# Kernel tuning notes

Measured on AMD Instinct MI355X. Metric: run time of the kernel, lower is better.

The kernel has to match this reference:

```python
import jax, jax.numpy as jnp
import numpy as np

IOU_THR = 0.5
SIGMA = 0.2
BETA = 0.6
EPS = 1e-8
SCORE_FLOOR = 0.01
N_BOXES = 8192
IMG = 640.0


def setup_inputs() -> dict:
    key = jax.random.key(0)
    k1, k2, k3 = jax.random.split(key, 3)
    # realistic detector output: centers in [0, 640], sizes in [5, 105]
    c = jax.random.uniform(k1, (N_BOXES, 2), dtype=jnp.float32) * IMG
    wh = jax.random.uniform(k2, (N_BOXES, 2), dtype=jnp.float32) * 100.0 + 5.0
    boxes = jnp.concatenate([c - wh / 2, c + wh / 2], axis=-1)  # [N,4] x1y1x2y2
    scores = jax.random.uniform(k3, (N_BOXES,), dtype=jnp.float32)
    return {"boxes": boxes, "scores": scores}


def pairwise_iou(b):
    # b: [N,4] -> [N,N]
    x1 = jnp.maximum(b[:, None, 0], b[None, :, 0])
    y1 = jnp.maximum(b[:, None, 1], b[None, :, 1])
    x2 = jnp.minimum(b[:, None, 2], b[None, :, 2])
    y2 = jnp.minimum(b[:, None, 3], b[None, :, 3])
    inter = jnp.clip(x2 - x1, 0) * jnp.clip(y2 - y1, 0)
    area = (b[:, 2] - b[:, 0]) * (b[:, 3] - b[:, 1])
    union = area[:, None] + area[None, :] - inter
    return inter / (union + EPS)


def diou_vec(b1, B):
    # b1: [4] pseudo-box, B: [N,4] pseudo-boxes -> DIoU [N]
    # (faithful to original: calculate_diou is called on rows of the IoU matrix,
    #  which only uses the first 4 columns as if they were box coords)
    x1 = jnp.maximum(b1[0], B[:, 0]); y1 = jnp.maximum(b1[1], B[:, 1])
    x2 = jnp.minimum(b1[2], B[:, 2]); y2 = jnp.minimum(b1[3], B[:, 3])
    inter = jnp.clip(x2 - x1, 0) * jnp.clip(y2 - y1, 0)
    a1 = (b1[2] - b1[0]) * (b1[3] - b1[1])
    a2 = (B[:, 2] - B[:, 0]) * (B[:, 3] - B[:, 1])
    iou = inter / (a1 + a2 - inter + EPS)
    cx1 = (b1[0] + b1[2]) / 2; cy1 = (b1[1] + b1[3]) / 2
    cx2 = (B[:, 0] + B[:, 2]) / 2; cy2 = (B[:, 1] + B[:, 3]) / 2
    cdist = (cx1 - cx2) ** 2 + (cy1 - cy2) ** 2
    ex1 = jnp.minimum(b1[0], B[:, 0]); ey1 = jnp.minimum(b1[1], B[:, 1])
    ex2 = jnp.maximum(b1[2], B[:, 2]); ey2 = jnp.maximum(b1[3], B[:, 3])
    edist = (ex2 - ex1) ** 2 + (ey2 - ey1) ** 2
    return iou - cdist / (edist + EPS)


def reference(boxes, scores):
    n = boxes.shape[0]
    order = jnp.argsort(-scores)              # descending score order
    b = boxes[order]
    s = scores[order]
    iou = pairwise_iou(b)                     # [N,N]
    iou_triu = iou * jnp.triu(jnp.ones((n, n), iou.dtype), k=1)
    pseudo = iou[:, :4]                       # rows of IoU matrix used as "boxes" (as in original)

    def body(carry, xs):
        keep, sc = carry
        row_triu, pbox, i = xs
        row_keep = keep[i]                    # skip row if already suppressed
        suppress = (row_triu > IOU_THR) & keep
        penalty = jnp.exp(-(row_triu ** 2) / SIGMA)
        diou = diou_vec(pbox, pseudo)
        total = jnp.minimum(penalty + diou ** 2 / BETA, 1.0)
        active = row_keep & suppress
        new_sc = jnp.where(active, sc * total, sc)
        new_keep = keep & ~(active & (new_sc < SCORE_FLOOR))
        return (new_keep, new_sc), None

    init = (jnp.ones(n, dtype=bool), s)
    (keep, sc), _ = jax.lax.scan(body, init, (iou_triu, pseudo, jnp.arange(n)))

    # map back to original index order
    scores_out = jnp.zeros_like(scores).at[order].set(sc)
    keep_out = jnp.zeros(n, dtype=bool).at[order].set(keep)
    return scores_out, keep_out
```

## Files before the change

### kernel.cpp

```cpp
#include <hip/hip_runtime.h>

#define N 8192
#define IOU_THR 0.5f
#define SIGMA 0.2f
#define BETA 0.6f
#define EPSF 1e-8f
#define SCORE_FLOOR 0.01f
#define NMS_T 1024
#define MAXS 20
#define PAIR_BUF 2048

__device__ __forceinline__ float iou_f(float4 a, float4 b) {
    float x1 = fmaxf(a.x, b.x);
    float y1 = fmaxf(a.y, b.y);
    float x2 = fminf(a.z, b.z);
    float y2 = fminf(a.w, b.w);
    float inter = fmaxf(x2 - x1, 0.0f) * fmaxf(y2 - y1, 0.0f);
    float aa = (a.z - a.x) * (a.w - a.y);
    float ab = (b.z - b.x) * (b.w - b.y);
    return inter / (aa + ab - inter + EPSF);
}

__device__ __forceinline__ float diou_f(float4 a, float4 b) {
    float x1 = fmaxf(a.x, b.x);
    float y1 = fmaxf(a.y, b.y);
    float x2 = fminf(a.z, b.z);
    float y2 = fminf(a.w, b.w);
    float inter = fmaxf(x2 - x1, 0.0f) * fmaxf(y2 - y1, 0.0f);
    float a1 = (a.z - a.x) * (a.w - a.y);
    float a2 = (b.z - b.x) * (b.w - b.y);
    float iou = inter / (a1 + a2 - inter + EPSF);
    float cx1 = (a.x + a.z) * 0.5f, cy1 = (a.y + a.w) * 0.5f;
    float cx2 = (b.x + b.z) * 0.5f, cy2 = (b.y + b.w) * 0.5f;
    float dx = cx1 - cx2, dy = cy1 - cy2;
    float cdist = dx * dx + dy * dy;
    float ex1 = fminf(a.x, b.x), ey1 = fminf(a.y, b.y);
    float ex2 = fmaxf(a.z, b.z), ey2 = fmaxf(a.w, b.w);
    float ew = ex2 - ex1, eh = ey2 - ey1;
    float edist = ew * ew + eh * eh;
    return iou - cdist / (edist + EPSF);
}

__global__ __launch_bounds__(256) void k_rank(const float* __restrict__ scores,
                                              int* __restrict__ rank) {
    __shared__ unsigned long long kj[256];
    int tid = threadIdx.x;
    int gj = blockIdx.x * 256 + tid;
    unsigned sbj = __float_as_uint(scores[gj]);
    kj[tid] = ((unsigned long long)(~sbj) << 32) | (unsigned)gj;
    __syncthreads();
    int gi = blockIdx.y * 256 + tid;
    unsigned sbi = __float_as_uint(scores[gi]);
    unsigned long long ki = ((unsigned long long)(~sbi) << 32) | (unsigned)gi;
    int cnt = 0;
#pragma unroll 8
    for (int q = 0; q < 256; ++q) cnt += (kj[q] < ki) ? 1 : 0;
    if (cnt) atomicAdd(&rank[gi], cnt);
}

__global__ __launch_bounds__(256) void k_scatter(const float4* __restrict__ boxes,
                                                 const float* __restrict__ scores,
                                                 const int* __restrict__ rank,
                                                 int* __restrict__ order,
                                                 float* __restrict__ s_sorted,
                                                 float4* __restrict__ b_sorted) {
    int t = blockIdx.x * 256 + threadIdx.x;
    int r = rank[t];
    order[r] = t;
    s_sorted[r] = scores[t];
    b_sorted[r] = boxes[t];
}

__global__ __launch_bounds__(256) void k_pairs(const float4* __restrict__ b,
                                               int* __restrict__ counter,
                                               int2* __restrict__ adj, int cap) {
    int tj = blockIdx.x, ti = blockIdx.y;
    if (tj < ti) return;
    __shared__ float4 bj[256];
    __shared__ float4 pj[256];
    __shared__ int2 lbuf[PAIR_BUF];
    __shared__ int lcount;
    __shared__ int lbase;
    int tid = threadIdx.x;
    if (tid == 0) lcount = 0;
    float4 t0 = b[0], t1 = b[1], t2 = b[2], t3 = b[3];
    int jbase = tj * 256;
    float4 bjv = b[jbase + tid];
    bj[tid] = bjv;
    float4 pjv;
    pjv.x = iou_f(bjv, t0);
    pjv.y = iou_f(bjv, t1);
    pjv.z = iou_f(bjv, t2);
    pjv.w = iou_f(bjv, t3);
    pj[tid] = pjv;
    __syncthreads();
    int i = ti * 256 + tid;
    float4 bi = b[i];
    float4 pi;
    pi.x = iou_f(bi, t0);
    pi.y = iou_f(bi, t1);
    pi.z = iou_f(bi, t2);
    pi.w = iou_f(bi, t3);
    for (int jj = 0; jj < 256; ++jj) {
        int j = jbase + jj;
        if (j <= i) continue;
        float v = iou_f(bi, bj[jj]);
        if (v > IOU_THR) {
            float penalty = expf(-(v * v) / SIGMA);
            float d = diou_f(pi, pj[jj]);
            float total = fminf(penalty + (d * d) / BETA, 1.0f);
            int pos = atomicAdd(&lcount, 1);
            if (pos < PAIR_BUF) {
                int2 e;
                e.x = (i << 13) | j;
                e.y = __float_as_int(total);
                lbuf[pos] = e;
            }
        }
    }
    __syncthreads();
    if (tid == 0) {
        int c = lcount;
        if (c > PAIR_BUF) c = PAIR_BUF;
        lcount = c;
        lbase = (c > 0) ? atomicAdd(counter, c) : 0;
    }
    __syncthreads();
    int c = lcount, base = lbase;
    for (int t = tid; t < c; t += 256) {
        int slot = base + t;
        if (slot < cap) adj[slot] = lbuf[t];
    }
}

__global__ __launch_bounds__(NMS_T) void k_nms(const int2* __restrict__ adj,
                                               const int* __restrict__ counter,
                                               const float* __restrict__ s_sorted,
                                               const int* __restrict__ order,
                                               float* __restrict__ out, int cap) {
    __shared__ float sc_l[N];
    __shared__ unsigned char keep_l[N];
    __shared__ unsigned int tag[N];
    int tid = threadIdx.x;
    for (int r = tid; r < N; r += NMS_T) {
        sc_l[r] = s_sorted[r];
        keep_l[r] = 1;
        tag[r] = 0u;
    }
    int T = counter[0];
    if (T > cap) T = cap;
    unsigned int ij[MAXS];
    float tot[MAXS];
    unsigned int mask = 0u;
#pragma unroll
    for (int s = 0; s < MAXS; ++s) {
        int g = s * NMS_T + tid;
        if (g < T) {
            int2 e = adj[g];
            ij[s] = (unsigned)e.x;
            tot[s] = __int_as_float(e.y);
            mask |= 1u << s;
        } else {
            ij[s] = 0u;
            tot[s] = 0.0f;
        }
    }
    unsigned int step = 0u;
    while (__syncthreads_count((int)(mask != 0u))) {
        ++step;
        unsigned int sv = step << 13;
#pragma unroll
        for (int s = 0; s < MAXS; ++s) {
            if (mask & (1u << s)) {
                unsigned int j_ = ij[s] & 8191u;
                unsigned int i_ = ij[s] >> 13;
                atomicMax(&tag[j_], sv | (8191u - i_));
            }
        }
        __syncthreads();
#pragma unroll
        for (int s = 0; s < MAXS; ++s) {
            if (mask & (1u << s)) {
                unsigned int i_ = ij[s] >> 13;
                unsigned int j_ = ij[s] & 8191u;
                unsigned int tgi = tag[i_];
                unsigned int tgj = tag[j_];
                if (((tgi >> 13) != step) && (tgj == (sv | (8191u - i_)))) {
                    if (keep_l[i_] && keep_l[j_]) {
                        float ns = sc_l[j_] * tot[s];
                        sc_l[j_] = ns;
                        if (ns < SCORE_FLOOR) keep_l[j_] = 0;
                    }
                    mask &= ~(1u << s);
                }
            }
        }
    }
    for (int r = tid; r < N; r += NMS_T) {
        int oi = order[r];
        out[oi] = sc_l[r];
        out[N + oi] = keep_l[r] ? 1.0f : 0.0f;
    }
}

extern "C" void kernel_launch(void* const* d_in, const int* in_sizes, int n_in,
                              void* d_out, int out_size, void* d_ws, size_t ws_size,
                              hipStream_t stream) {
    const float4* boxes = (const float4*)d_in[0];
    const float* scores = (const float*)d_in[1];
    float* out = (float*)d_out;
    char* ws = (char*)d_ws;

    int* order = (int*)(ws);
    float* s_sorted = (float*)(ws + (32 << 10));
    float4* b_sorted = (float4*)(ws + (64 << 10));
    int* rank = (int*)(ws + (192 << 10));
    int* counter = (int*)(ws + (224 << 10));
    int2* adj = (int2*)(ws + (256 << 10));

    long long cap_ll = ((long long)ws_size - (256 << 10)) / 8;
    if (cap_ll < 0) cap_ll = 0;
    if (cap_ll > (long long)NMS_T * MAXS) cap_ll = (long long)NMS_T * MAXS;
    int cap = (int)cap_ll;

    hipMemsetAsync(ws + (192 << 10), 0, 64 << 10, stream);
    hipLaunchKernelGGL(k_rank, dim3(32, 32), dim3(256), 0, stream, scores, rank);
    hipLaunchKernelGGL(k_scatter, dim3(32), dim3(256), 0, stream, boxes, scores, rank,
                       order, s_sorted, b_sorted);
    hipLaunchKernelGGL(k_pairs, dim3(32, 32), dim3(256), 0, stream, b_sorted, counter, adj, cap);
    hipLaunchKernelGGL(k_nms, dim3(1), dim3(NMS_T), 0, stream, adj, counter, s_sorted, order, out, cap);
}
```

Before: 215.2 us.

## Fuse rank, scatter, pair and NMS stages into one cooperative kernel

Replaces the memset and four separate launches with a single cooperative kernel of 256 blocks of 512 threads. Stages are separated by grid-wide syncs, and the upper-triangular tile pairs are enumerated with a linear index so that no block sits idle. The NMS phase now runs in one 512-thread block with up to 40 pair slots per thread, and it re-reads pair entries from global memory each step instead of holding them in registers. This removes launch and memset overhead, at the cost of grid-sync latency, a smaller NMS block, and extra global loads inside the serial NMS loop.

```diff
diff --git a/kernel.cpp b/kernel.cpp
--- a/kernel.cpp
+++ b/kernel.cpp
@@ -1,4 +1,7 @@
 #include <hip/hip_runtime.h>
+#include <hip/hip_cooperative_groups.h>
+
+namespace cg = cooperative_groups;
 
 #define N 8192
 #define IOU_THR 0.5f
@@ -6,8 +9,10 @@
 #define BETA 0.6f
 #define EPSF 1e-8f
 #define SCORE_FLOOR 0.01f
-#define NMS_T 1024
-#define MAXS 20
+#define NBLK 256
+#define NTHR 512
+#define MAXS 40
+#define CAP (NTHR * MAXS)
 #define PAIR_BUF 2048
 
 __device__ __forceinline__ float iou_f(float4 a, float4 b) {
@@ -41,165 +46,170 @@
     return iou - cdist / (edist + EPSF);
 }
 
-__global__ __launch_bounds__(256) void k_rank(const float* __restrict__ scores,
-                                              int* __restrict__ rank) {
-    __shared__ unsigned long long kj[256];
+__global__ __launch_bounds__(NTHR) void k_fused(const float4* __restrict__ boxes,
+                                                const float* __restrict__ scores,
+                                                float* __restrict__ out,
+                                                int* __restrict__ rank,
+                                                int* __restrict__ order,
+                                                float* __restrict__ s_sorted,
+                                                float4* __restrict__ b_sorted,
+                                                int2* __restrict__ adj, int cap) {
+    cg::grid_group grid = cg::this_grid();
+    __shared__ __align__(16) char smem[73728];
+    __shared__ int lcount, lbase;
     int tid = threadIdx.x;
-    int gj = blockIdx.x * 256 + tid;
-    unsigned sbj = __float_as_uint(scores[gj]);
-    kj[tid] = ((unsigned long long)(~sbj) << 32) | (unsigned)gj;
-    __syncthreads();
-    int gi = blockIdx.y * 256 + tid;
-    unsigned sbi = __float_as_uint(scores[gi]);
-    unsigned long long ki = ((unsigned long long)(~sbi) << 32) | (unsigned)gi;
-    int cnt = 0;
+    int b = blockIdx.x;
+
+    {
+        int idx = b * NTHR + tid;
+        if (idx <= N) rank[idx] = 0;
+    }
+    grid.sync();
+
+    {
+        unsigned long long* kj = (unsigned long long*)smem;
+        int it = b >> 4, jt = b & 15;
+        int gj = jt * NTHR + tid;
+        unsigned sbj = __float_as_uint(scores[gj]);
+        kj[tid] = ((unsigned long long)(~sbj) << 32) | (unsigned)gj;
+        __syncthreads();
+        int gi = it * NTHR + tid;
+        unsigned sbi = __float_as_uint(scores[gi]);
+        unsigned long long ki = ((unsigned long long)(~sbi) << 32) | (unsigned)gi;
+        int cnt = 0;
 #pragma unroll 8
-    for (int q = 0; q < 256; ++q) cnt += (kj[q] < ki) ? 1 : 0;
-    if (cnt) atomicAdd(&rank[gi], cnt);
-}
-
-__global__ __launch_bounds__(256) void k_scatter(const float4* __restrict__ boxes,
-                                                 const float* __restrict__ scores,
-                                                 const int* __restrict__ rank,
-                                                 int* __restrict__ order,
-                                                 float* __restrict__ s_sorted,
-                                                 float4* __restrict__ b_sorted) {
-    int t = blockIdx.x * 256 + threadIdx.x;
-    int r = rank[t];
-    order[r] = t;
-    s_sorted[r] = scores[t];
-    b_sorted[r] = boxes[t];
-}
-
-__global__ __launch_bounds__(256) void k_pairs(const float4* __restrict__ b,
-                                               int* __restrict__ counter,
-                                               int2* __restrict__ adj, int cap) {
-    int tj = blockIdx.x, ti = blockIdx.y;
-    if (tj < ti) return;
-    __shared__ float4 bj[256];
-    __shared__ float4 pj[256];
-    __shared__ int2 lbuf[PAIR_BUF];
-    __shared__ int lcount;
-    __shared__ int lbase;
-    int tid = threadIdx.x;
-    if (tid == 0) lcount = 0;
-    float4 t0 = b[0], t1 = b[1], t2 = b[2], t3 = b[3];
-    int jbase = tj * 256;
-    float4 bjv = b[jbase + tid];
-    bj[tid] = bjv;
-    float4 pjv;
-    pjv.x = iou_f(bjv, t0);
-    pjv.y = iou_f(bjv, t1);
-    pjv.z = iou_f(bjv, t2);
-    pjv.w = iou_f(bjv, t3);
-    pj[tid] = pjv;
-    __syncthreads();
-    int i = ti * 256 + tid;
-    float4 bi = b[i];
-    float4 pi;
-    pi.x = iou_f(bi, t0);
-    pi.y = iou_f(bi, t1);
-    pi.z = iou_f(bi, t2);
-    pi.w = iou_f(bi, t3);
-    for (int jj = 0; jj < 256; ++jj) {
-        int j = jbase + jj;
-        if (j <= i) continue;
-        float v = iou_f(bi, bj[jj]);
-        if (v > IOU_THR) {
-            float penalty = expf(-(v * v) / SIGMA);
-            float d = diou_f(pi, pj[jj]);
-            float total = fminf(penalty + (d * d) / BETA, 1.0f);
-            int pos = atomicAdd(&lcount, 1);
-            if (pos < PAIR_BUF) {
-                int2 e;
-                e.x = (i << 13) | j;
-                e.y = __float_as_int(total);
-                lbuf[pos] = e;
-            }
-        }
-    }
-    __syncthreads();
-    if (tid == 0) {
-        int c = lcount;
-        if (c > PAIR_BUF) c = PAIR_BUF;
-        lcount = c;
-        lbase = (c > 0) ? atomicAdd(counter, c) : 0;
-    }
-    __syncthreads();
-    int c = lcount, base = lbase;
-    for (int t = tid; t < c; t += 256) {
-        int slot = base + t;
-        if (slot < cap) adj[slot] = lbuf[t];
-    }
-}
-
-__global__ __launch_bounds__(NMS_T) void k_nms(const int2* __restrict__ adj,
-                                               const int* __restrict__ counter,
-                                               const float* __restrict__ s_sorted,
-                                               const int* __restrict__ order,
-                                               float* __restrict__ out, int cap) {
-    __shared__ float sc_l[N];
-    __shared__ unsigned char keep_l[N];
-    __shared__ unsigned int tag[N];
-    int tid = threadIdx.x;
-    for (int r = tid; r < N; r += NMS_T) {
-        sc_l[r] = s_sorted[r];
-        keep_l[r] = 1;
-        tag[r] = 0u;
-    }
-    int T = counter[0];
-    if (T > cap) T = cap;
-    unsigned int ij[MAXS];
-    float tot[MAXS];
-    unsigned int mask = 0u;
+        for (int q = 0; q < NTHR; ++q) cnt += (kj[q] < ki) ? 1 : 0;
+        if (cnt) atomicAdd(&rank[gi], cnt);
+        __syncthreads();
+    }
+    grid.sync();
+
+    if (b < 16) {
+        int t = b * NTHR + tid;
+        int r = rank[t];
+        order[r] = t;
+        s_sorted[r] = scores[t];
+        b_sorted[r] = boxes[t];
+    }
+    grid.sync();
+
+    {
+        float4* bj = (float4*)smem;
+        float4* pj = (float4*)(smem + 4096);
+        int2* lbuf = (int2*)(smem + 8192);
+        float4 t0 = b_sorted[0], t1 = b_sorted[1], t2 = b_sorted[2], t3 = b_sorted[3];
+        for (int L = b; L < 528; L += NBLK) {
+            int ti = 0, off = 0;
+            while (off + (32 - ti) <= L) { off += 32 - ti; ++ti; }
+            int tj = ti + (L - off);
+            __syncthreads();
+            if (tid == 0) lcount = 0;
+            if (tid < 256) {
+                float4 bv = b_sorted[tj * 256 + tid];
+                bj[tid] = bv;
+                float4 pv;
+                pv.x = iou_f(bv, t0); pv.y = iou_f(bv, t1);
+                pv.z = iou_f(bv, t2); pv.w = iou_f(bv, t3);
+                pj[tid] = pv;
+            }
+            __syncthreads();
+            int ii = tid & 255;
+            int half = tid >> 8;
+            int i = ti * 256 + ii;
+            float4 bi = b_sorted[i];
+            float4 pi;
+            pi.x = iou_f(bi, t0); pi.y = iou_f(bi, t1);
+            pi.z = iou_f(bi, t2); pi.w = iou_f(bi, t3);
+            int j0 = half * 128, j1 = j0 + 128;
+            for (int jj = j0; jj < j1; ++jj) {
+                int j = tj * 256 + jj;
+                if (j <= i) continue;
+                float v = iou_f(bi, bj[jj]);
+                if (v > IOU_THR) {
+                    float penalty = expf(-(v * v) / SIGMA);
+                    float d = diou_f(pi, pj[jj]);
+                    float total = fminf(penalty + (d * d) / BETA, 1.0f);
+                    int pos = atomicAdd(&lcount, 1);
+                    if (pos < PAIR_BUF) {
+                        int2 e;
+                        e.x = (i << 13) | j;
+                        e.y = __float_as_int(total);
+                        lbuf[pos] = e;
+                    }
+                }
+            }
+            __syncthreads();
+            if (tid == 0) {
+                int c = lcount;
+                if (c > PAIR_BUF) c = PAIR_BUF;
+                lcount = c;
+                lbase = c ? atomicAdd(&rank[N], c) : 0;
+            }
+            __syncthreads();
+            int c = lcount, base = lbase;
+            for (int t = tid; t < c; t += NTHR) {
+                int slot = base + t;
+                if (slot < cap) adj[slot] = lbuf[t];
+            }
+        }
+    }
+    grid.sync();
+
+    if (b != 0) return;
+    {
+        float* sc_l = (float*)smem;
+        unsigned char* keep_l = (unsigned char*)(smem + 32768);
+        unsigned int* tag = (unsigned int*)(smem + 40960);
+        for (int r = tid; r < N; r += NTHR) {
+            sc_l[r] = s_sorted[r];
+            keep_l[r] = 1;
+            tag[r] = 0u;
+        }
+        __syncthreads();
+        int T = rank[N];
+        if (T > cap) T = cap;
+        unsigned long long mask = 0ull;
 #pragma unroll
-    for (int s = 0; s < MAXS; ++s) {
-        int g = s * NMS_T + tid;
-        if (g < T) {
-            int2 e = adj[g];
-            ij[s] = (unsigned)e.x;
-            tot[s] = __int_as_float(e.y);
-            mask |= 1u << s;
-        } else {
-            ij[s] = 0u;
-            tot[s] = 0.0f;
-        }
-    }
-    unsigned int step = 0u;
-    while (__syncthreads_count((int)(mask != 0u))) {
-        ++step;
-        unsigned int sv = step << 13;
+        for (int s = 0; s < MAXS; ++s)
+            if (s * NTHR + tid < T) mask |= 1ull << s;
+        unsigned int step = 0u;
+        while (__syncthreads_count((int)(mask != 0ull))) {
+            ++step;
+            unsigned int sv = step << 13;
 #pragma unroll
-        for (int s = 0; s < MAXS; ++s) {
-            if (mask & (1u << s)) {
-                unsigned int j_ = ij[s] & 8191u;
-                unsigned int i_ = ij[s] >> 13;
-                atomicMax(&tag[j_], sv | (8191u - i_));
-            }
-        }
-        __syncthreads();
+            for (int s = 0; s < MAXS; ++s) {
+                if (mask & (1ull << s)) {
+                    int2 e = adj[s * NTHR + tid];
+                    unsigned int i_ = ((unsigned)e.x) >> 13;
+                    unsigned int j_ = ((unsigned)e.x) & 8191u;
+                    atomicMax(&tag[j_], sv | (8191u - i_));
+                }
+            }
+            __syncthreads();
 #pragma unroll
-        for (int s = 0; s < MAXS; ++s) {
-            if (mask & (1u << s)) {
-                unsigned int i_ = ij[s] >> 13;
-                unsigned int j_ = ij[s] & 8191u;
-                unsigned int tgi = tag[i_];
-                unsigned int tgj = tag[j_];
-                if (((tgi >> 13) != step) && (tgj == (sv | (8191u - i_)))) {
-                    if (keep_l[i_] && keep_l[j_]) {
-                        float ns = sc_l[j_] * tot[s];
-                        sc_l[j_] = ns;
-                        if (ns < SCORE_FLOOR) keep_l[j_] = 0;
+            for (int s = 0; s < MAXS; ++s) {
+                if (mask & (1ull << s)) {
+                    int2 e = adj[s * NTHR + tid];
+                    unsigned int i_ = ((unsigned)e.x) >> 13;
+                    unsigned int j_ = ((unsigned)e.x) & 8191u;
+                    unsigned int tgi = tag[i_];
+                    unsigned int tgj = tag[j_];
+                    if (((tgi >> 13) != step) && (tgj == (sv | (8191u - i_)))) {
+                        if (keep_l[i_] && keep_l[j_]) {
+                            float ns = sc_l[j_] * __int_as_float(e.y);
+                            sc_l[j_] = ns;
+                            if (ns < SCORE_FLOOR) keep_l[j_] = 0;
+                        }
+                        mask &= ~(1ull << s);
                     }
-                    mask &= ~(1u << s);
                 }
             }
         }
-    }
-    for (int r = tid; r < N; r += NMS_T) {
-        int oi = order[r];
-        out[oi] = sc_l[r];
-        out[N + oi] = keep_l[r] ? 1.0f : 0.0f;
+        for (int r = tid; r < N; r += NTHR) {
+            int oi = order[r];
+            out[oi] = sc_l[r];
+            out[N + oi] = keep_l[r] ? 1.0f : 0.0f;
+        }
     }
 }
 
@@ -211,22 +221,20 @@
     float* out = (float*)d_out;
     char* ws = (char*)d_ws;
 
-    int* order = (int*)(ws);
-    float* s_sorted = (float*)(ws + (32 << 10));
-    float4* b_sorted = (float4*)(ws + (64 << 10));
-    int* rank = (int*)(ws + (192 << 10));
-    int* counter = (int*)(ws + (224 << 10));
-    int2* adj = (int2*)(ws + (256 << 10));
-
-    long long cap_ll = ((long long)ws_size - (256 << 10)) / 8;
-    if (cap_ll < 0) cap_ll = 0;
-    if (cap_ll > (long long)NMS_T * MAXS) cap_ll = (long long)NMS_T * MAXS;
-    int cap = (int)cap_ll;
-
-    hipMemsetAsync(ws + (192 << 10), 0, 64 << 10, stream);
-    hipLaunchKernelGGL(k_rank, dim3(32, 32), dim3(256), 0, stream, scores, rank);
-    hipLaunchKernelGGL(k_scatter, dim3(32), dim3(256), 0, stream, boxes, scores, rank,
-                       order, s_sorted, b_sorted);
-    hipLaunchKernelGGL(k_pairs, dim3(32, 32), dim3(256), 0, stream, b_sorted, counter, adj, cap);
-    hipLaunchKernelGGL(k_nms, dim3(1), dim3(NMS_T), 0, stream, adj, counter, s_sorted, order, out, cap);
-}
+    int* rank = (int*)ws;
+    int* order = (int*)(ws + (36 << 10));
+    float* s_sorted = (float*)(ws + (68 << 10));
+    float4* b_sorted = (float4*)(ws + (100 << 10));
+    int2* adj = (int2*)(ws + (228 << 10));
+
+    int cap = CAP;
+    long long avail = ((long long)ws_size - (228 << 10)) / 8;
+    if (avail < 0) avail = 0;
+    if (avail < cap) cap = (int)avail;
+
+    void* args[] = {(void*)&boxes, (void*)&scores, (void*)&out, (void*)&rank,
+                    (void*)&order, (void*)&s_sorted, (void*)&b_sorted,
+                    (void*)&adj, (void*)&cap};
+    hipLaunchCooperativeKernel((const void*)k_fused, dim3(NBLK), dim3(NTHR),
+                               args, 0, stream);
+}
```

Result: slower. 415.8 us (+93.3%).

## Fuse rank+scatter, drop memset, and solve NMS via fixed-point keep iteration

Applied to the files above, without the earlier changes.

Merges the rank-counting and scatter kernels into one kernel that computes each box's sorted position directly and also zeroes the pair counter, which removes the memset and a launch. The NMS kernel first iterates a parallel fixed point: it multiplies all penalties from kept suppressors into each target's score and recomputes keep flags until nothing changes. After that, only edges into suppressed boxes are replayed in the ordered tag-based loop to reproduce exact score products. This cuts the serialized step count, but adds float CAS loops, up to 64 global passes and changed multiplication order, so results may differ slightly.

```diff
diff --git a/kernel.cpp b/kernel.cpp
--- a/kernel.cpp
+++ b/kernel.cpp
@@ -6,9 +6,10 @@
 #define BETA 0.6f
 #define EPSF 1e-8f
 #define SCORE_FLOOR 0.01f
+#define PAIR_BUF 2048
 #define NMS_T 1024
-#define MAXS 20
-#define PAIR_BUF 2048
+#define SLOTS 20
+#define CAPMAX (NMS_T * SLOTS)
 
 __device__ __forceinline__ float iou_f(float4 a, float4 b) {
     float x1 = fmaxf(a.x, b.x);
@@ -41,34 +42,38 @@
     return iou - cdist / (edist + EPSF);
 }
 
-__global__ __launch_bounds__(256) void k_rank(const float* __restrict__ scores,
-                                              int* __restrict__ rank) {
-    __shared__ unsigned long long kj[256];
-    int tid = threadIdx.x;
-    int gj = blockIdx.x * 256 + tid;
-    unsigned sbj = __float_as_uint(scores[gj]);
-    kj[tid] = ((unsigned long long)(~sbj) << 32) | (unsigned)gj;
-    __syncthreads();
-    int gi = blockIdx.y * 256 + tid;
-    unsigned sbi = __float_as_uint(scores[gi]);
-    unsigned long long ki = ((unsigned long long)(~sbi) << 32) | (unsigned)gi;
-    int cnt = 0;
-#pragma unroll 8
-    for (int q = 0; q < 256; ++q) cnt += (kj[q] < ki) ? 1 : 0;
-    if (cnt) atomicAdd(&rank[gi], cnt);
-}
-
-__global__ __launch_bounds__(256) void k_scatter(const float4* __restrict__ boxes,
+__global__ __launch_bounds__(512) void k_ranksct(const float4* __restrict__ boxes,
                                                  const float* __restrict__ scores,
-                                                 const int* __restrict__ rank,
                                                  int* __restrict__ order,
                                                  float* __restrict__ s_sorted,
-                                                 float4* __restrict__ b_sorted) {
-    int t = blockIdx.x * 256 + threadIdx.x;
-    int r = rank[t];
-    order[r] = t;
-    s_sorted[r] = scores[t];
-    b_sorted[r] = boxes[t];
+                                                 float4* __restrict__ b_sorted,
+                                                 int* __restrict__ counter) {
+    __shared__ int psum[64][8];
+    int tid = threadIdx.x;
+    int il = tid >> 3, sub = tid & 7;
+    int i = blockIdx.x * 64 + il;
+    float si = scores[i];
+    const float4* s4 = (const float4*)scores;
+    int c0 = sub * 256;
+    int cnt = 0;
+    for (int c = c0; c < c0 + 256; ++c) {
+        float4 v = s4[c];
+        int j0 = c * 4;
+        cnt += (v.x > si) || ((v.x == si) && (j0 < i));
+        cnt += (v.y > si) || ((v.y == si) && (j0 + 1 < i));
+        cnt += (v.z > si) || ((v.z == si) && (j0 + 2 < i));
+        cnt += (v.w > si) || ((v.w == si) && (j0 + 3 < i));
+    }
+    psum[il][sub] = cnt;
+    __syncthreads();
+    if (sub == 0) {
+        int r = psum[il][0] + psum[il][1] + psum[il][2] + psum[il][3]
+              + psum[il][4] + psum[il][5] + psum[il][6] + psum[il][7];
+        order[r] = i;
+        s_sorted[r] = si;
+        b_sorted[r] = boxes[i];
+    }
+    if (blockIdx.x == 0 && tid == 0) counter[0] = 0;
 }
 
 __global__ __launch_bounds__(256) void k_pairs(const float4* __restrict__ b,
@@ -79,8 +84,7 @@
     __shared__ float4 bj[256];
     __shared__ float4 pj[256];
     __shared__ int2 lbuf[PAIR_BUF];
-    __shared__ int lcount;
-    __shared__ int lbase;
+    __shared__ int lcount, lbase;
     int tid = threadIdx.x;
     if (tid == 0) lcount = 0;
     float4 t0 = b[0], t1 = b[1], t2 = b[2], t3 = b[3];
@@ -88,19 +92,15 @@
     float4 bjv = b[jbase + tid];
     bj[tid] = bjv;
     float4 pjv;
-    pjv.x = iou_f(bjv, t0);
-    pjv.y = iou_f(bjv, t1);
-    pjv.z = iou_f(bjv, t2);
-    pjv.w = iou_f(bjv, t3);
+    pjv.x = iou_f(bjv, t0); pjv.y = iou_f(bjv, t1);
+    pjv.z = iou_f(bjv, t2); pjv.w = iou_f(bjv, t3);
     pj[tid] = pjv;
     __syncthreads();
     int i = ti * 256 + tid;
     float4 bi = b[i];
     float4 pi;
-    pi.x = iou_f(bi, t0);
-    pi.y = iou_f(bi, t1);
-    pi.z = iou_f(bi, t2);
-    pi.w = iou_f(bi, t3);
+    pi.x = iou_f(bi, t0); pi.y = iou_f(bi, t1);
+    pi.z = iou_f(bi, t2); pi.w = iou_f(bi, t3);
     for (int jj = 0; jj < 256; ++jj) {
         int j = jbase + jj;
         if (j <= i) continue;
@@ -123,7 +123,7 @@
         int c = lcount;
         if (c > PAIR_BUF) c = PAIR_BUF;
         lcount = c;
-        lbase = (c > 0) ? atomicAdd(counter, c) : 0;
+        lbase = c ? atomicAdd(counter, c) : 0;
     }
     __syncthreads();
     int c = lcount, base = lbase;
@@ -138,58 +138,100 @@
                                                const float* __restrict__ s_sorted,
                                                const int* __restrict__ order,
                                                float* __restrict__ out, int cap) {
-    __shared__ float sc_l[N];
-    __shared__ unsigned char keep_l[N];
-    __shared__ unsigned int tag[N];
+    __shared__ float s_l[N];
+    __shared__ float prod[N];
+    __shared__ unsigned char keepA[N];
+    __shared__ unsigned char keepB[N];
+    __shared__ unsigned int touched[N / 32];
     int tid = threadIdx.x;
     for (int r = tid; r < N; r += NMS_T) {
-        sc_l[r] = s_sorted[r];
-        keep_l[r] = 1;
-        tag[r] = 0u;
+        s_l[r] = s_sorted[r];
+        keepA[r] = 1;
     }
     int T = counter[0];
     if (T > cap) T = cap;
-    unsigned int ij[MAXS];
-    float tot[MAXS];
+
+    for (int iter = 0; iter < 64; ++iter) {
+        __syncthreads();
+        for (int r = tid; r < N; r += NMS_T) prod[r] = s_l[r];
+        if (tid < N / 32) touched[tid] = 0u;
+        __syncthreads();
+#pragma unroll
+        for (int s = 0; s < SLOTS; ++s) {
+            int g = s * NMS_T + tid;
+            if (g < T) {
+                int2 e = adj[g];
+                int i_ = ((unsigned)e.x) >> 13;
+                int j_ = e.x & 8191;
+                if (keepA[i_]) {
+                    atomicOr(&touched[j_ >> 5], 1u << (j_ & 31));
+                    unsigned* up = (unsigned*)&prod[j_];
+                    float f = __int_as_float(e.y);
+                    unsigned cur = *(volatile unsigned*)up, assumed;
+                    do {
+                        assumed = cur;
+                        cur = atomicCAS(up, assumed,
+                                        __float_as_uint(__uint_as_float(assumed) * f));
+                    } while (cur != assumed);
+                }
+            }
+        }
+        __syncthreads();
+        int mychange = 0;
+        for (int r = tid; r < N; r += NMS_T) {
+            bool t_ = (touched[r >> 5] >> (r & 31)) & 1u;
+            unsigned char nk = (t_ && prod[r] < SCORE_FLOOR) ? 0 : 1;
+            mychange |= (nk != keepA[r]);
+            keepB[r] = nk;
+        }
+        int changed = __syncthreads_count(mychange);
+        for (int r = tid; r < N; r += NMS_T) keepA[r] = keepB[r];
+        if (changed == 0) break;
+    }
+
+    for (int r = tid; r < N; r += NMS_T) {
+        if (!keepA[r]) { prod[r] = s_l[r]; keepB[r] = 0; }
+    }
+    __syncthreads();
+    unsigned int* tag = (unsigned int*)s_l;
+    for (int r = tid; r < N; r += NMS_T) tag[r] = 0u;
+
     unsigned int mask = 0u;
 #pragma unroll
-    for (int s = 0; s < MAXS; ++s) {
+    for (int s = 0; s < SLOTS; ++s) {
         int g = s * NMS_T + tid;
         if (g < T) {
             int2 e = adj[g];
-            ij[s] = (unsigned)e.x;
-            tot[s] = __int_as_float(e.y);
-            mask |= 1u << s;
-        } else {
-            ij[s] = 0u;
-            tot[s] = 0.0f;
+            int i_ = ((unsigned)e.x) >> 13;
+            int j_ = e.x & 8191;
+            if (keepA[i_] && !keepA[j_]) mask |= 1u << s;
         }
     }
     unsigned int step = 0u;
-    while (__syncthreads_count((int)(mask != 0u))) {
+    while (step < 4096u && __syncthreads_count((int)(mask != 0u))) {
         ++step;
         unsigned int sv = step << 13;
 #pragma unroll
-        for (int s = 0; s < MAXS; ++s) {
+        for (int s = 0; s < SLOTS; ++s) {
             if (mask & (1u << s)) {
-                unsigned int j_ = ij[s] & 8191u;
-                unsigned int i_ = ij[s] >> 13;
+                int2 e = adj[s * NMS_T + tid];
+                unsigned i_ = ((unsigned)e.x) >> 13;
+                unsigned j_ = ((unsigned)e.x) & 8191u;
                 atomicMax(&tag[j_], sv | (8191u - i_));
             }
         }
         __syncthreads();
 #pragma unroll
-        for (int s = 0; s < MAXS; ++s) {
+        for (int s = 0; s < SLOTS; ++s) {
             if (mask & (1u << s)) {
-                unsigned int i_ = ij[s] >> 13;
-                unsigned int j_ = ij[s] & 8191u;
-                unsigned int tgi = tag[i_];
-                unsigned int tgj = tag[j_];
-                if (((tgi >> 13) != step) && (tgj == (sv | (8191u - i_)))) {
-                    if (keep_l[i_] && keep_l[j_]) {
-                        float ns = sc_l[j_] * tot[s];
-                        sc_l[j_] = ns;
-                        if (ns < SCORE_FLOOR) keep_l[j_] = 0;
+                int2 e = adj[s * NMS_T + tid];
+                unsigned i_ = ((unsigned)e.x) >> 13;
+                unsigned j_ = ((unsigned)e.x) & 8191u;
+                if (tag[j_] == (sv | (8191u - i_))) {
+                    if (!keepB[j_]) {
+                        float ns = prod[j_] * __int_as_float(e.y);
+                        prod[j_] = ns;
+                        if (ns < SCORE_FLOOR) keepB[j_] = 1;
                     }
                     mask &= ~(1u << s);
                 }
@@ -198,8 +240,8 @@
     }
     for (int r = tid; r < N; r += NMS_T) {
         int oi = order[r];
-        out[oi] = sc_l[r];
-        out[N + oi] = keep_l[r] ? 1.0f : 0.0f;
+        out[oi] = prod[r];
+        out[N + oi] = keepA[r] ? 1.0f : 0.0f;
     }
 }
 
@@ -214,19 +256,18 @@
     int* order = (int*)(ws);
     float* s_sorted = (float*)(ws + (32 << 10));
     float4* b_sorted = (float4*)(ws + (64 << 10));
-    int* rank = (int*)(ws + (192 << 10));
-    int* counter = (int*)(ws + (224 << 10));
-    int2* adj = (int2*)(ws + (256 << 10));
-
-    long long cap_ll = ((long long)ws_size - (256 << 10)) / 8;
-    if (cap_ll < 0) cap_ll = 0;
-    if (cap_ll > (long long)NMS_T * MAXS) cap_ll = (long long)NMS_T * MAXS;
-    int cap = (int)cap_ll;
-
-    hipMemsetAsync(ws + (192 << 10), 0, 64 << 10, stream);
-    hipLaunchKernelGGL(k_rank, dim3(32, 32), dim3(256), 0, stream, scores, rank);
-    hipLaunchKernelGGL(k_scatter, dim3(32), dim3(256), 0, stream, boxes, scores, rank,
-                       order, s_sorted, b_sorted);
-    hipLaunchKernelGGL(k_pairs, dim3(32, 32), dim3(256), 0, stream, b_sorted, counter, adj, cap);
-    hipLaunchKernelGGL(k_nms, dim3(1), dim3(NMS_T), 0, stream, adj, counter, s_sorted, order, out, cap);
-}
+    int* counter = (int*)(ws + (192 << 10));
+    int2* adj = (int2*)(ws + (196 << 10));
+
+    long long avail = ((long long)ws_size - (196 << 10)) / 8;
+    if (avail < 0) avail = 0;
+    int cap = CAPMAX;
+    if (avail < cap) cap = (int)avail;
+
+    hipLaunchKernelGGL(k_ranksct, dim3(128), dim3(512), 0, stream,
+                       boxes, scores, order, s_sorted, b_sorted, counter);
+    hipLaunchKernelGGL(k_pairs, dim3(32, 32), dim3(256), 0, stream,
+                       b_sorted, counter, adj, cap);
+    hipLaunchKernelGGL(k_nms, dim3(1), dim3(NMS_T), 0, stream,
+                       adj, counter, s_sorted, order, out, cap);
+}
```

Result: slower. 276.0 us (+28.3%).

## Replace edge-tag NMS loop with CSR-grouped fixed-point resolution per box

Applied to the files above, without the earlier changes.

The single-block NMS kernel now builds a CSR adjacency, grouping suppression pairs by target box through a shared-memory histogram, prefix scan and scatter. It then resolves keep/suppress state with a fixed-point iteration: a box is decided once all of its suppressors are decided. This replaces the per-step atomicMax tagging over edges that serialized one suppression per target per step. Scores and keep flags are written straight to the output as boxes are decided. The edge cap rises to 16384 and the block shrinks to 512 threads. Risks: the decision rule may not match sequential semantics for every input, the iteration count depends on chain depth, and the inner loops over each box's edges diverge across threads.

```diff
diff --git a/kernel.cpp b/kernel.cpp
--- a/kernel.cpp
+++ b/kernel.cpp
@@ -6,9 +6,8 @@
 #define BETA 0.6f
 #define EPSF 1e-8f
 #define SCORE_FLOOR 0.01f
-#define NMS_T 1024
-#define MAXS 20
 #define PAIR_BUF 2048
+#define TCAP 16384
 
 __device__ __forceinline__ float iou_f(float4 a, float4 b) {
     float x1 = fmaxf(a.x, b.x);
@@ -79,8 +78,7 @@
     __shared__ float4 bj[256];
     __shared__ float4 pj[256];
     __shared__ int2 lbuf[PAIR_BUF];
-    __shared__ int lcount;
-    __shared__ int lbase;
+    __shared__ int lcount, lbase;
     int tid = threadIdx.x;
     if (tid == 0) lcount = 0;
     float4 t0 = b[0], t1 = b[1], t2 = b[2], t3 = b[3];
@@ -88,19 +86,15 @@
     float4 bjv = b[jbase + tid];
     bj[tid] = bjv;
     float4 pjv;
-    pjv.x = iou_f(bjv, t0);
-    pjv.y = iou_f(bjv, t1);
-    pjv.z = iou_f(bjv, t2);
-    pjv.w = iou_f(bjv, t3);
+    pjv.x = iou_f(bjv, t0); pjv.y = iou_f(bjv, t1);
+    pjv.z = iou_f(bjv, t2); pjv.w = iou_f(bjv, t3);
     pj[tid] = pjv;
     __syncthreads();
     int i = ti * 256 + tid;
     float4 bi = b[i];
     float4 pi;
-    pi.x = iou_f(bi, t0);
-    pi.y = iou_f(bi, t1);
-    pi.z = iou_f(bi, t2);
-    pi.w = iou_f(bi, t3);
+    pi.x = iou_f(bi, t0); pi.y = iou_f(bi, t1);
+    pi.z = iou_f(bi, t2); pi.w = iou_f(bi, t3);
     for (int jj = 0; jj < 256; ++jj) {
         int j = jbase + jj;
         if (j <= i) continue;
@@ -123,7 +117,7 @@
         int c = lcount;
         if (c > PAIR_BUF) c = PAIR_BUF;
         lcount = c;
-        lbase = (c > 0) ? atomicAdd(counter, c) : 0;
+        lbase = c ? atomicAdd(counter, c) : 0;
     }
     __syncthreads();
     int c = lcount, base = lbase;
@@ -133,73 +127,104 @@
     }
 }
 
-__global__ __launch_bounds__(NMS_T) void k_nms(const int2* __restrict__ adj,
-                                               const int* __restrict__ counter,
-                                               const float* __restrict__ s_sorted,
-                                               const int* __restrict__ order,
-                                               float* __restrict__ out, int cap) {
-    __shared__ float sc_l[N];
-    __shared__ unsigned char keep_l[N];
-    __shared__ unsigned int tag[N];
+__global__ __launch_bounds__(512) void k_nms(const int2* __restrict__ adj,
+                                             const int* __restrict__ counter,
+                                             const float* __restrict__ s_sorted,
+                                             const int* __restrict__ order,
+                                             float* __restrict__ out, int cap) {
+    __shared__ unsigned short idx16[TCAP];
+    __shared__ float fac[TCAP];
+    __shared__ int starts[N];
+    __shared__ unsigned char state[N];
+    __shared__ int wsum[8];
     int tid = threadIdx.x;
-    for (int r = tid; r < N; r += NMS_T) {
-        sc_l[r] = s_sorted[r];
-        keep_l[r] = 1;
-        tag[r] = 0u;
-    }
     int T = counter[0];
     if (T > cap) T = cap;
-    unsigned int ij[MAXS];
-    float tot[MAXS];
-    unsigned int mask = 0u;
-#pragma unroll
-    for (int s = 0; s < MAXS; ++s) {
-        int g = s * NMS_T + tid;
+    if (T > TCAP) T = TCAP;
+
+    for (int r = tid; r < N; r += 512) { starts[r] = 0; state[r] = 0; }
+    __syncthreads();
+
+    for (int s = 0; s < 32; ++s) {
+        int g = s * 512 + tid;
         if (g < T) {
             int2 e = adj[g];
-            ij[s] = (unsigned)e.x;
-            tot[s] = __int_as_float(e.y);
-            mask |= 1u << s;
-        } else {
-            ij[s] = 0u;
-            tot[s] = 0.0f;
-        }
-    }
-    unsigned int step = 0u;
-    while (__syncthreads_count((int)(mask != 0u))) {
-        ++step;
-        unsigned int sv = step << 13;
+            atomicAdd(&starts[e.x & 8191], 1);
+        }
+    }
+    __syncthreads();
+
+    int loc[16];
+    int base = tid * 16;
+    int sum = 0;
 #pragma unroll
-        for (int s = 0; s < MAXS; ++s) {
-            if (mask & (1u << s)) {
-                unsigned int j_ = ij[s] & 8191u;
-                unsigned int i_ = ij[s] >> 13;
-                atomicMax(&tag[j_], sv | (8191u - i_));
+    for (int q = 0; q < 16; ++q) { loc[q] = starts[base + q]; sum += loc[q]; }
+    int lane = tid & 63, wv = tid >> 6;
+    int v = sum;
+    for (int off = 1; off < 64; off <<= 1) {
+        int u = __shfl_up(v, off);
+        if (lane >= off) v += u;
+    }
+    if (lane == 63) wsum[wv] = v;
+    __syncthreads();
+    if (tid < 8) {
+        int x = wsum[tid];
+        for (int off = 1; off < 8; off <<= 1) {
+            int u = __shfl_up(x, off);
+            if (tid >= off) x += u;
+        }
+        wsum[tid] = x;
+    }
+    __syncthreads();
+    int excl = ((wv == 0) ? 0 : wsum[wv - 1]) + (v - sum);
+#pragma unroll
+    for (int q = 0; q < 16; ++q) { starts[base + q] = excl; excl += loc[q]; }
+    __syncthreads();
+
+    for (int s = 0; s < 32; ++s) {
+        int g = s * 512 + tid;
+        if (g < T) {
+            int2 e = adj[g];
+            int j = e.x & 8191;
+            int i = ((unsigned)e.x) >> 13;
+            int pos = atomicAdd(&starts[j], 1);
+            idx16[pos] = (unsigned short)i;
+            fac[pos] = __int_as_float(e.y);
+        }
+    }
+
+    int iter = 0;
+    while (true) {
+        __syncthreads();
+        int undec = 0;
+        for (int k = 0; k < 16; ++k) {
+            int j = k * 512 + tid;
+            if (state[j]) continue;
+            int s0 = j ? starts[j - 1] : 0;
+            int s1 = starts[j];
+            float P = s_sorted[j];
+            bool any = false, unk = false;
+            for (int e = s0; e < s1; ++e) {
+                unsigned char st = state[idx16[e]];
+                if (st == 1) { P *= fac[e]; any = true; }
+                else if (st == 0) { unk = true; }
             }
-        }
-        __syncthreads();
-#pragma unroll
-        for (int s = 0; s < MAXS; ++s) {
-            if (mask & (1u << s)) {
-                unsigned int i_ = ij[s] >> 13;
-                unsigned int j_ = ij[s] & 8191u;
-                unsigned int tgi = tag[i_];
-                unsigned int tgj = tag[j_];
-                if (((tgi >> 13) != step) && (tgj == (sv | (8191u - i_)))) {
-                    if (keep_l[i_] && keep_l[j_]) {
-                        float ns = sc_l[j_] * tot[s];
-                        sc_l[j_] = ns;
-                        if (ns < SCORE_FLOOR) keep_l[j_] = 0;
-                    }
-                    mask &= ~(1u << s);
-                }
+            if (any && P < SCORE_FLOOR) {
+                state[j] = 2;
+                int oi = order[j];
+                out[oi] = P;
+                out[N + oi] = 0.0f;
+            } else if (!unk) {
+                state[j] = 1;
+                int oi = order[j];
+                out[oi] = P;
+                out[N + oi] = 1.0f;
+            } else {
+                ++undec;
             }
         }
-    }
-    for (int r = tid; r < N; r += NMS_T) {
-        int oi = order[r];
-        out[oi] = sc_l[r];
-        out[N + oi] = keep_l[r] ? 1.0f : 0.0f;
+        if (__syncthreads_count(undec) == 0) break;
+        if (++iter > 4096) break;
     }
 }
 
@@ -218,15 +243,15 @@
     int* counter = (int*)(ws + (224 << 10));
     int2* adj = (int2*)(ws + (256 << 10));
 
-    long long cap_ll = ((long long)ws_size - (256 << 10)) / 8;
-    if (cap_ll < 0) cap_ll = 0;
-    if (cap_ll > (long long)NMS_T * MAXS) cap_ll = (long long)NMS_T * MAXS;
-    int cap = (int)cap_ll;
+    long long avail = ((long long)ws_size - (256 << 10)) / 8;
+    if (avail < 0) avail = 0;
+    int cap = TCAP;
+    if (avail < cap) cap = (int)avail;
 
     hipMemsetAsync(ws + (192 << 10), 0, 64 << 10, stream);
     hipLaunchKernelGGL(k_rank, dim3(32, 32), dim3(256), 0, stream, scores, rank);
     hipLaunchKernelGGL(k_scatter, dim3(32), dim3(256), 0, stream, boxes, scores, rank,
                        order, s_sorted, b_sorted);
     hipLaunchKernelGGL(k_pairs, dim3(32, 32), dim3(256), 0, stream, b_sorted, counter, adj, cap);
-    hipLaunchKernelGGL(k_nms, dim3(1), dim3(NMS_T), 0, stream, adj, counter, s_sorted, order, out, cap);
-}
+    hipLaunchKernelGGL(k_nms, dim3(1), dim3(512), 0, stream, adj, counter, s_sorted, order, out, cap);
+}
```

Measured after the change: 239.4 us. 11.3% more time.
